# Performance work log

Measured on AMD Instinct MI355X. Metric: run time of the kernel, lower is better.

## Reference

```python
import jax, jax.numpy as jnp
import numpy as np

IMG_H, IMG_W = 800, 1216
STRIDE = 16
SIZES = (128.0, 256.0, 512.0)
RATIOS = (0.5, 1.0, 2.0)
NMS_THRESH = 0.7
MIN_SIZE = 16.0
PRE_NMS = 6000   # testing mode
POST_NMS = 300   # testing mode


def _base_anchors():
    # torchvision-style: ratio = h/w, anchors centered at origin, xyxy
    base = []
    for s in SIZES:
        for r in RATIOS:
            hr = np.sqrt(r)
            w, h = s / hr, s * hr
            base.append([-w / 2.0, -h / 2.0, w / 2.0, h / 2.0])
    return jnp.asarray(np.array(base, dtype=np.float32))  # [A,4]


def _anchors(H, W):
    base = _base_anchors()                                  # [A,4]
    sx = jnp.arange(W, dtype=jnp.float32) * STRIDE
    sy = jnp.arange(H, dtype=jnp.float32) * STRIDE
    shift_x, shift_y = jnp.meshgrid(sx, sy)                 # [H,W] each
    shifts = jnp.stack([shift_x, shift_y, shift_x, shift_y], axis=-1)
    # row-major over (h, w), anchors innermost -> matches permute(0,2,3,1) layout
    return (shifts.reshape(-1, 1, 4) + base[None]).reshape(-1, 4)  # [H*W*A,4]


def _conv(x, w, b, pad):
    y = jax.lax.conv_general_dilated(x, w, (1, 1), pad,
                                     dimension_numbers=('NCHW', 'OIHW', 'NCHW'))
    return y + b[None, :, None, None]


def _decode(deltas, anchors):
    wa = anchors[:, 2] - anchors[:, 0]
    ha = anchors[:, 3] - anchors[:, 1]
    cxa = anchors[:, 0] + 0.5 * wa
    cya = anchors[:, 1] + 0.5 * ha
    cx = deltas[:, 0] * wa + cxa
    cy = deltas[:, 1] * ha + cya
    w = jnp.exp(deltas[:, 2]) * wa
    h = jnp.exp(deltas[:, 3]) * ha
    return jnp.stack([cx - 0.5 * w, cy - 0.5 * h, cx + 0.5 * w, cy + 0.5 * h], axis=-1)


def _nms(boxes, scores):
    # boxes: [N,4] sorted by descending score; greedy IoU-suppression NMS
    N = boxes.shape[0]
    areas = (boxes[:, 2] - boxes[:, 0]) * (boxes[:, 3] - boxes[:, 1])

    def body(i, st):
        sup, kidx, kval = st
        avail = jnp.where(sup, -jnp.inf, scores)
        j = jnp.argmax(avail)
        valid = avail[j] > -jnp.inf
        b = boxes[j]
        ix1 = jnp.maximum(b[0], boxes[:, 0])
        iy1 = jnp.maximum(b[1], boxes[:, 1])
        ix2 = jnp.minimum(b[2], boxes[:, 2])
        iy2 = jnp.minimum(b[3], boxes[:, 3])
        inter = jnp.clip(ix2 - ix1, 0.0) * jnp.clip(iy2 - iy1, 0.0)
        union = areas[j] + areas - inter
        iou = jnp.where(union > 0, inter / union, 0.0)
        sup2 = (sup | (iou > NMS_THRESH)).at[j].set(True)
        sup = jnp.where(valid, sup2, sup.at[j].set(True))
        return sup, kidx.at[i].set(j), kval.at[i].set(valid)

    sup0 = jnp.zeros((N,), jnp.bool_)
    _, kidx, kval = jax.lax.fori_loop(
        0, POST_NMS, body,
        (sup0, jnp.zeros((POST_NMS,), jnp.int32), jnp.zeros((POST_NMS,), jnp.bool_)))
    # fixed-size output [POST_NMS,4]; invalid slots zeroed
    return boxes[kidx] * kval[:, None].astype(boxes.dtype)


def setup_inputs() -> dict:
    key = jax.random.key(0)
    ks = jax.random.split(key, 4)
    return {
        'features': jax.random.normal(ks[0], (8, 512, 50, 76), jnp.float32),
        'conv_w': 0.01 * jax.random.normal(ks[1], (512, 512, 3, 3), jnp.float32),
        'conv_b': jnp.zeros((512,), jnp.float32),
        'cls_w': 0.01 * jax.random.normal(ks[2], (9, 512, 1, 1), jnp.float32),
        'cls_b': jnp.zeros((9,), jnp.float32),
        'box_w': 0.01 * jax.random.normal(ks[3], (36, 512, 1, 1), jnp.float32),
        'box_b': jnp.zeros((36,), jnp.float32),
    }


def reference(features, conv_w, conv_b, cls_w, cls_b, box_w, box_b):
    B, _, H, W = features.shape
    t = jax.nn.relu(_conv(features, conv_w, conv_b, 'SAME'))
    obj = _conv(t, cls_w, cls_b, 'VALID')                     # [B,A,H,W]
    objectness = jnp.transpose(obj, (0, 2, 3, 1)).reshape(B, -1)        # [B,N]
    bd = _conv(t, box_w, box_b, 'VALID')                      # [B,4A,H,W]
    bbox_deltas = jnp.transpose(bd, (0, 2, 3, 1)).reshape(B, -1, 4)     # [B,N,4]
    anchors = _anchors(H, W)                                  # [N,4]

    def per_image(scores, deltas):
        props = _decode(deltas, anchors)
        props = jnp.stack([jnp.clip(props[:, 0], 0.0, IMG_W),
                           jnp.clip(props[:, 1], 0.0, IMG_H),
                           jnp.clip(props[:, 2], 0.0, IMG_W),
                           jnp.clip(props[:, 3], 0.0, IMG_H)], axis=-1)
        keep = ((props[:, 2] - props[:, 0]) >= MIN_SIZE) & \
               ((props[:, 3] - props[:, 1]) >= MIN_SIZE)
        s = jnp.where(keep, scores, -jnp.inf)  # small boxes never selected
        top_s, top_i = jax.lax.top_k(s, PRE_NMS)
        return _nms(props[top_i], top_s)

    proposals = jax.vmap(per_image)(objectness, bbox_deltas)  # [B,POST_NMS,4]
    return proposals, objectness, bbox_deltas
```

## Files before the change

### kernel.cpp

```cpp
#include <hip/hip_runtime.h>
#include <stdint.h>
#include <math.h>

typedef unsigned int u32;
typedef unsigned long long u64;
typedef double d4 __attribute__((ext_vector_type(4)));
typedef _Float16 h8 __attribute__((ext_vector_type(8)));
typedef float f32x16 __attribute__((ext_vector_type(16)));

#define NPX    3800
#define NANCH  34200
#define NSEL   6000
#define NOUT   300
#define NPXP   4160

#define OFF_T        0ull
#define OFF_WTH      62259200ull
#define OFF_WTL      66977792ull
#define OFF_BOXES    71696384ull
#define OFF_ITEMS    76073984ull
#define OFF_FSPH     78262784ull
#define OFF_FSPL     112341504ull
#define WS_NEED_F16  146551296ull
#define OFF_PART     OFF_FSPH
#define WS_NEED_SPLITK (OFF_PART + 43776000ull)

#define GLL16(gsrc, ldst) \
    __builtin_amdgcn_global_load_lds((const __attribute__((address_space(1))) void*)(gsrc), \
                                     (__attribute__((address_space(3))) void*)(ldst), 16, 0, 0)

__global__ __launch_bounds__(256) void zero_kernel(float4* __restrict__ p, unsigned n) {
    unsigned i = blockIdx.x * 256u + threadIdx.x;
    const unsigned stride = gridDim.x * 256u;
    const float4 z = make_float4(0.f, 0.f, 0.f, 0.f);
    for (; i < n; i += stride) p[i] = z;
}

__global__ __launch_bounds__(256) void wsplit_kernel(const float* __restrict__ cw,
                                                     _Float16* __restrict__ wh,
                                                     _Float16* __restrict__ wl) {
    int o = blockIdx.x * 256 + threadIdx.x;
    if (o >= 9 * 512 * 512) return;
    int ci = o & 511;
    int co = (o >> 9) & 511;
    int kk = o >> 18;
    float v = cw[(((co << 9) + ci) * 9) + kk] * 1024.0f;
    _Float16 h = (_Float16)v;
    float r = v - (float)h;
    wh[o] = h;
    wl[o] = (_Float16)r;
}

__global__ __launch_bounds__(256) void fsplit_kernel(const float* __restrict__ feat,
                                                     _Float16* __restrict__ fh,
                                                     _Float16* __restrict__ fl) {
    const int b = blockIdx.z, ci0 = blockIdx.y << 5, p0 = blockIdx.x << 6;
    const int tid = threadIdx.x;
    __shared__ __align__(16) _Float16 shh[64][32];
    __shared__ __align__(16) _Float16 shl[64][32];
    {
        const int r = tid >> 3, xg = tid & 7;
        const int p = p0 + (xg << 3);
        float v[8];
        if (p < NPX) {
            const float* sp = feat + ((size_t)(b * 512 + ci0 + r)) * NPX + p;
            #pragma unroll
            for (int j = 0; j < 8; ++j) v[j] = sp[j];
        } else {
            #pragma unroll
            for (int j = 0; j < 8; ++j) v[j] = 0.f;
        }
        #pragma unroll
        for (int j = 0; j < 8; ++j) {
            float s = v[j] * 512.0f;
            _Float16 h = (_Float16)s;
            float rr = s - (float)h;
            shh[(xg << 3) + j][r] = h;
            shl[(xg << 3) + j][r] = (_Float16)rr;
        }
    }
    __syncthreads();
    {
        const int px = tid >> 2, cg = tid & 3;
        const int p = p0 + px;
        if (p < NPX) {
            const int yy = p / 76, xx = p - yy * 76;
            const size_t dst = ((size_t)b * NPXP + (size_t)((yy + 1) * 80 + xx + 2)) * 512
                             + ci0 + (cg << 3);
            *(h8*)(fh + dst) = *(const h8*)&shh[px][cg << 3];
            *(h8*)(fl + dst) = *(const h8*)&shl[px][cg << 3];
        }
    }
}

__global__ __launch_bounds__(256, 2) void conv3x3_f16_kernel(
    const _Float16* __restrict__ fh, const _Float16* __restrict__ fl,
    const _Float16* __restrict__ wh, const _Float16* __restrict__ wl,
    const float* __restrict__ bias, float* __restrict__ t)
{
    const int id  = blockIdx.x;
    const int b   = id & 7;
    const int g   = id >> 3;
    const int co0 = (g & 3) << 7;
    const int pt0 = (g >> 2) << 7;
    const int tid = threadIdx.x;
    const int w   = tid >> 6;
    const int l   = tid & 63;
    const int wm  = w >> 1, wn = w & 1;
    const int ln  = l & 31, lk = l >> 5;

    __shared__ __align__(16) _Float16 S[2][16][512];

    const _Float16* sb[4];
    u32 ldof[4];
    const long long fbase = (long long)b * NPXP + pt0;
    #pragma unroll
    for (int i = 0; i < 4; ++i) {
        const int ti = (w << 2) + i;
        ldof[i] = (u32)(ti * 1024 + l * 16);
        if (ti < 8) {
            const int mtile = ti >> 1, hl = ti & 1;
            sb[i] = (hl ? wl : wh) + ((long long)(co0 + (mtile << 5) + ln) << 9) + (lk << 3);
        } else {
            const int tj = ti - 8;
            const int ntile = tj >> 1, hl = tj & 1;
            sb[i] = (hl ? fl : fh) + ((fbase + (ntile << 5) + ln) << 9) + (lk << 3);
        }
    }
    char* lbase = (char*)&S[0][0][0];

    auto stage = [&](int q, int db) {
        const int kk  = q >> 5;
        const int ci0 = (q & 31) << 4;
        long long off;
        if (w < 2) {
            off = ((long long)kk << 18) + ci0;
        } else {
            const int kd = (kk * 11) >> 5;
            const int s  = kd * 77 + kk - 81;
            off = ((long long)s << 9) + ci0;
        }
        char* ld = lbase + (db << 14);
        #pragma unroll
        for (int i = 0; i < 4; ++i)
            GLL16(sb[i] + off, ld + ldof[i]);
    };

    f32x16 acc[2][2], l2[2][2];
    #pragma unroll
    for (int i = 0; i < 2; ++i)
        #pragma unroll
        for (int j = 0; j < 2; ++j)
            #pragma unroll
            for (int gg = 0; gg < 16; ++gg) { acc[i][j][gg] = 0.0f; l2[i][j][gg] = 0.0f; }

    stage(0, 0);
    __syncthreads();

    const int ao = l << 3;

    for (int q = 0; q < 288; ++q) {
        const int db = q & 1;
        if (q < 287) stage(q + 1, db ^ 1);
        const _Float16* Sq = &S[db][0][0];
        h8 Ah[2], Al[2], Bh[2], Bl[2];
        #pragma unroll
        for (int i = 0; i < 2; ++i) {
            const int mtile = (wm << 1) + i;
            const int ntile = (wn << 1) + i;
            Ah[i] = *(const h8*)(Sq + ((mtile << 1) + 0) * 512 + ao);
            Al[i] = *(const h8*)(Sq + ((mtile << 1) + 1) * 512 + ao);
            Bh[i] = *(const h8*)(Sq + ((8 + (ntile << 1)) + 0) * 512 + ao);
            Bl[i] = *(const h8*)(Sq + ((8 + (ntile << 1)) + 1) * 512 + ao);
        }
        #pragma unroll
        for (int i = 0; i < 2; ++i)
            #pragma unroll
            for (int j = 0; j < 2; ++j) {
                acc[i][j] = __builtin_amdgcn_mfma_f32_32x32x16_f16(Ah[i], Bh[j], acc[i][j], 0, 0, 0);
                acc[i][j] = __builtin_amdgcn_mfma_f32_32x32x16_f16(Ah[i], Bl[j], acc[i][j], 0, 0, 0);
                acc[i][j] = __builtin_amdgcn_mfma_f32_32x32x16_f16(Al[i], Bh[j], acc[i][j], 0, 0, 0);
            }
        if ((q & 7) == 7) {
            #pragma unroll
            for (int i = 0; i < 2; ++i)
                #pragma unroll
                for (int j = 0; j < 2; ++j) {
                    l2[i][j] += acc[i][j];
                    #pragma unroll
                    for (int gg = 0; gg < 16; ++gg) acc[i][j][gg] = 0.0f;
                }
        }
        if (q < 287) __syncthreads();
    }

    int rcp[16];
    {
        h8 pa, pb;
        #pragma unroll
        for (int j = 0; j < 8; ++j) { pa[j] = (_Float16)(float)ln; pb[j] = (_Float16)0.0625f; }
        f32x16 pr, pc;
        #pragma unroll
        for (int gg = 0; gg < 16; ++gg) { pr[gg] = 0.0f; pc[gg] = 0.0f; }
        pr = __builtin_amdgcn_mfma_f32_32x32x16_f16(pa, pb, pr, 0, 0, 0);
        pc = __builtin_amdgcn_mfma_f32_32x32x16_f16(pb, pa, pc, 0, 0, 0);
        #pragma unroll
        for (int gg = 0; gg < 16; ++gg)
            rcp[gg] = ((int)(pr[gg] + 0.5f)) | (((int)(pc[gg] + 0.5f)) << 8);
    }

    const double dsc = 1.0 / 524288.0;
    #pragma unroll
    for (int i = 0; i < 2; ++i) {
        #pragma unroll
        for (int j = 0; j < 2; ++j) {
            #pragma unroll
            for (int gg = 0; gg < 16; ++gg) {
                const int row = rcp[gg] & 255;
                const int col = rcp[gg] >> 8;
                const int co  = co0 + (wm << 6) + (i << 5) + row;
                const int pp  = pt0 + (wn << 6) + (j << 5) + col;
                const int yy  = pp / 80;
                const int xx  = pp - yy * 80;
                if (yy >= 1 && yy < 51 && xx >= 2 && xx < 78) {
                    const double v = (double)l2[i][j][gg] * dsc + (double)bias[co];
                    t[((size_t)(b * 512 + co)) * NPX + (yy - 1) * 76 + (xx - 2)]
                        = (float)(v > 0.0 ? v : 0.0);
                }
            }
        }
    }
}

__global__ __launch_bounds__(1024) void wtrans_kernel(const float* __restrict__ cw,
                                                      float* __restrict__ wt) {
    int o = blockIdx.x * 1024 + threadIdx.x;
    if (o >= 512*512*9) return;
    int co = o & 511;
    int ci = (o >> 9) & 511;
    int kk = o >> 18;
    wt[o] = cw[((co << 9) + ci) * 9 + kk];
}

__global__ __launch_bounds__(256, 2) void conv3x3_mfma_kernel(const float* __restrict__ feat,
                                                              const float* __restrict__ wt,
                                                              const float* __restrict__ bias,
                                                              float* __restrict__ t) {
    const int b   = blockIdx.z;
    const int co0 = blockIdx.y << 7;
    const int px0 = blockIdx.x << 6;
    const int tid = threadIdx.x;
    const int w    = tid >> 6;
    const int l    = tid & 63;
    const int quad = l >> 4;
    const int lc   = l & 15;

    __shared__ double BsF[2][1024];

    int rr[4], cc[4];
    {
        d4 pzr = {0.0, 0.0, 0.0, 0.0};
        d4 pzc = {0.0, 0.0, 0.0, 0.0};
        double paM = (double)lc;
        double pbN = (double)lc;
        pzr = __builtin_amdgcn_mfma_f64_16x16x4f64(paM, 1.0, pzr, 0, 0, 0);
        pzc = __builtin_amdgcn_mfma_f64_16x16x4f64(1.0, pbN, pzc, 0, 0, 0);
        #pragma unroll
        for (int g = 0; g < 4; ++g) {
            rr[g] = (((int)pzr[g]) >> 2) & 15;
            cc[g] = (((int)pzc[g]) >> 2) & 15;
        }
    }

    d4 acc[2][4];
    #pragma unroll
    for (int i = 0; i < 2; ++i)
        #pragma unroll
        for (int j = 0; j < 4; ++j) acc[i][j] = (d4){0.0, 0.0, 0.0, 0.0};

    const float* featb = feat + (size_t)b * 512 * NPX;

    const int b_quad = (tid >> 4) & 3;
    const int b_pxl  = ((tid >> 6) << 4) | (tid & 15);
    const int p      = px0 + b_pxl;
    const int py     = p / 76;
    const int px     = p - py * 76;
    const bool pvalid = (p < NPX);

    float vaf[8], vbf[4];
    double a_cur[8];

    auto loadA = [&](int q, float* va) {
        int kk  = q >> 5;
        int ci0 = (q & 31) << 4;
        const float* ap = wt + (((size_t)(kk * 512 + ci0 + quad)) << 9)
                             + co0 + (w << 5) + lc;
        #pragma unroll
        for (int ks = 0; ks < 4; ++ks) {
            va[ks * 2 + 0] = ap[(ks << 11)];
            va[ks * 2 + 1] = ap[(ks << 11) + 16];
        }
    };
    auto loadB = [&](int q, float* vb) {
        int kk  = q >> 5;
        int ci0 = (q & 31) << 4;
        int kd = kk / 3;
        int dy = kd - 1, dx = kk - kd * 3 - 1;
        int iy = py + dy, ix = px + dx;
        bool ok = pvalid && ((unsigned)iy < 50u) && ((unsigned)ix < 76u);
        if (ok) {
            const float* bp = featb + (size_t)(ci0 + b_quad) * NPX + iy * 76 + ix;
            #pragma unroll
            for (int j = 0; j < 4; ++j) vb[j] = bp[(size_t)(j << 2) * NPX];
        } else {
            vb[0] = vb[1] = vb[2] = vb[3] = 0.0f;
        }
    };

    loadA(0, vaf); loadB(0, vbf);
    #pragma unroll
    for (int j = 0; j < 4; ++j) BsF[0][tid + (j << 8)] = (double)vbf[j];
    #pragma unroll
    for (int j = 0; j < 8; ++j) a_cur[j] = (double)vaf[j];
    __syncthreads();

    for (int q = 0; q < 288; ++q) {
        const int cur = q & 1;
        if (q < 287) { loadA(q + 1, vaf); loadB(q + 1, vbf); }
        const double* bb = BsF[cur];
        #pragma unroll
        for (int ks = 0; ks < 4; ++ks) {
            const double* bp = bb + (ks << 8);
            double a0 = a_cur[ks * 2], a1 = a_cur[ks * 2 + 1];
            #pragma unroll
            for (int nt = 0; nt < 4; ++nt) {
                double bv = bp[(nt << 6) + l];
                acc[0][nt] = __builtin_amdgcn_mfma_f64_16x16x4f64(a0, bv, acc[0][nt], 0, 0, 0);
                acc[1][nt] = __builtin_amdgcn_mfma_f64_16x16x4f64(a1, bv, acc[1][nt], 0, 0, 0);
            }
        }
        if (q < 287) {
            #pragma unroll
            for (int j = 0; j < 4; ++j) BsF[cur ^ 1][tid + (j << 8)] = (double)vbf[j];
            #pragma unroll
            for (int j = 0; j < 8; ++j) a_cur[j] = (double)vaf[j];
            __syncthreads();
        }
    }

    #pragma unroll
    for (int mt = 0; mt < 2; ++mt) {
        #pragma unroll
        for (int g = 0; g < 4; ++g) {
            int co = co0 + (w << 5) + (mt << 4) + rr[g];
            double bs = (double)bias[co];
            float* row = t + ((size_t)b * 512 + co) * NPX;
            #pragma unroll
            for (int nt = 0; nt < 4; ++nt) {
                int pp = px0 + (nt << 4) + cc[g];
                if (pp < NPX) {
                    double v = acc[mt][nt][g] + bs;
                    row[pp] = (float)(v > 0.0 ? v : 0.0);
                }
            }
        }
    }
}

__global__ __launch_bounds__(64) void heads_partial_kernel(const float* __restrict__ t,
                                                           const float* __restrict__ cls_w,
                                                           const float* __restrict__ box_w,
                                                           double* __restrict__ part) {
    const int b = blockIdx.y, c = blockIdx.z;
    const int p = blockIdx.x * 64 + threadIdx.x;
    if (p >= NPX) return;
    const float* tb = t + ((size_t)b * 512 + c * 128) * NPX + p;

    double ac[9]  = {};
    double ab[36] = {};
    for (int ci = 0; ci < 128; ++ci) {
        double tv = (double)tb[(size_t)ci * NPX];
        int cw = c * 128 + ci;
        #pragma unroll
        for (int o = 0; o < 9;  ++o) ac[o] = fma((double)cls_w[o * 512 + cw], tv, ac[o]);
        #pragma unroll
        for (int o = 0; o < 36; ++o) ab[o] = fma((double)box_w[o * 512 + cw], tv, ab[o]);
    }
    double* dst = part + ((size_t)(c * 8 + b) * 45) * NPX + p;
    #pragma unroll
    for (int o = 0; o < 9;  ++o) dst[(size_t)o * NPX] = ac[o];
    #pragma unroll
    for (int o = 0; o < 36; ++o) dst[(size_t)(9 + o) * NPX] = ab[o];
}

__device__ __forceinline__ void decode_px(int b, int p, const double* s45,
                                          const float* cls_b, const float* box_b,
                                          float* out_obj, float* out_del,
                                          float* boxes, u64* items) {
    float* ob = out_obj + (size_t)b * NANCH + (size_t)p * 9;
    float* dl = out_del + (size_t)b * NANCH * 4 + (size_t)p * 36;
    const int yy = p / 76, xx = p - yy * 76;

    #pragma unroll
    for (int a = 0; a < 9; ++a) {
        double s  = s45[a] + (double)cls_b[a];
        ob[a] = (float)s;
        double d0 = s45[9 + 4*a + 0] + (double)box_b[4*a+0];
        double d1 = s45[9 + 4*a + 1] + (double)box_b[4*a+1];
        double d2 = s45[9 + 4*a + 2] + (double)box_b[4*a+2];
        double d3 = s45[9 + 4*a + 3] + (double)box_b[4*a+3];
        dl[4*a+0] = (float)d0; dl[4*a+1] = (float)d1;
        dl[4*a+2] = (float)d2; dl[4*a+3] = (float)d3;

        int si = a / 3, ri = a - si * 3;
        double sz = (si == 0) ? 128.0 : ((si == 1) ? 256.0 : 512.0);
        double hr = (ri == 0) ? 0.7071067811865476 : ((ri == 1) ? 1.0 : 1.4142135623730951);
        float bx2f = (float)(sz / hr * 0.5);
        float by2f = (float)(sz * hr * 0.5);

        double sx = (double)(xx * 16), sy = (double)(yy * 16);
        double x1 = sx - (double)bx2f, x2 = sx + (double)bx2f;
        double y1 = sy - (double)by2f, y2 = sy + (double)by2f;

        double wa = x2 - x1, ha = y2 - y1;
        double cxa = x1 + 0.5 * wa, cya = y1 + 0.5 * ha;
        double cx = d0 * wa + cxa, cy = d1 * ha + cya;
        double w  = exp(d2) * wa,  h  = exp(d3) * ha;

        double px1 = cx - 0.5 * w, py1 = cy - 0.5 * h;
        double px2 = cx + 0.5 * w, py2 = cy + 0.5 * h;
        px1 = fmin(fmax(px1, 0.0), 1216.0);
        py1 = fmin(fmax(py1, 0.0), 800.0);
        px2 = fmin(fmax(px2, 0.0), 1216.0);
        py2 = fmin(fmax(py2, 0.0), 800.0);

        bool keep = ((px2 - px1) >= 16.0) && ((py2 - py1) >= 16.0);
        double se = keep ? s : -INFINITY;

        u64 ubits = (u64)__double_as_longlong(se);
        u64 ka = (ubits >> 63) ? ~ubits : (ubits | 0x8000000000000000ull);
        u64 kd = ~ka;
        int n = p * 9 + a;
        items[(size_t)b * NANCH + n] = (kd & ~0xFFFFull) | (u64)(u32)n;
        *(float4*)(boxes + ((size_t)b * NANCH + n) * 4) =
            make_float4((float)px1, (float)py1, (float)px2, (float)py2);
    }
}

__global__ __launch_bounds__(64) void reduce_decode_kernel(const double* __restrict__ part,
                                                           const float* __restrict__ cls_b,
                                                           const float* __restrict__ box_b,
                                                           float* __restrict__ out_obj,
                                                           float* __restrict__ out_del,
                                                           float* __restrict__ boxes,
                                                           u64* __restrict__ items) {
    const int b = blockIdx.y;
    const int p = blockIdx.x * 64 + threadIdx.x;
    if (p >= NPX) return;
    double s45[45];
    #pragma unroll
    for (int o = 0; o < 45; ++o) {
        double s = part[((size_t)(0 * 8 + b) * 45 + o) * NPX + p];
        s += part[((size_t)(1 * 8 + b) * 45 + o) * NPX + p];
        s += part[((size_t)(2 * 8 + b) * 45 + o) * NPX + p];
        s += part[((size_t)(3 * 8 + b) * 45 + o) * NPX + p];
        s45[o] = s;
    }
    decode_px(b, p, s45, cls_b, box_b, out_obj, out_del, boxes, items);
}

__global__ __launch_bounds__(256) void heads_decode_kernel(const float* __restrict__ t,
                                                           const float* __restrict__ cls_w,
                                                           const float* __restrict__ cls_b,
                                                           const float* __restrict__ box_w,
                                                           const float* __restrict__ box_b,
                                                           float* __restrict__ out_obj,
                                                           float* __restrict__ out_del,
                                                           float* __restrict__ boxes,
                                                           u64* __restrict__ items) {
    const int b = blockIdx.y;
    const int p = blockIdx.x * 256 + threadIdx.x;
    if (p >= NPX) return;
    const float* tb = t + (size_t)b * 512 * NPX + p;
    double s45[45];
    #pragma unroll
    for (int o = 0; o < 45; ++o) s45[o] = 0.0;
    for (int ci = 0; ci < 512; ++ci) {
        double tv = (double)tb[(size_t)ci * NPX];
        #pragma unroll
        for (int o = 0; o < 9;  ++o) s45[o]     = fma((double)cls_w[o * 512 + ci], tv, s45[o]);
        #pragma unroll
        for (int o = 0; o < 36; ++o) s45[9 + o] = fma((double)box_w[o * 512 + ci], tv, s45[9 + o]);
    }
    decode_px(b, p, s45, cls_b, box_b, out_obj, out_del, boxes, items);
}

__device__ __forceinline__ bool iou_gt(float4 A, float4 B, float areaA, float areaB) {
    float ix1 = fmaxf(A.x, B.x), iy1 = fmaxf(A.y, B.y);
    float ix2 = fminf(A.z, B.z), iy2 = fminf(A.w, B.w);
    float iw = fmaxf(ix2 - ix1, 0.0f), ih = fmaxf(iy2 - iy1, 0.0f);
    float inter = iw * ih;
    float uni = areaA + areaB - inter;
    float iou = (uni > 0.0f) ? (inter / uni) : 0.0f;
    return iou > 0.7f;
}

__global__ __launch_bounds__(1024) void topk_nms_kernel(const u64* __restrict__ items,
                                                        const float* __restrict__ boxes,
                                                        float* __restrict__ out) {
    extern __shared__ u64 buf[];
    u32* hist = (u32*)buf;
    u32* scan = hist + 4096;
    u32* scal = hist + 5120;

    const int b   = blockIdx.x;
    const int tid = threadIdx.x;
    const u64* it = items + (size_t)b * NANCH;

    #pragma unroll
    for (int i = 0; i < 4; ++i) hist[tid * 4 + i] = 0;
    __syncthreads();
    for (int i = tid; i < NANCH; i += 1024)
        atomicAdd(&hist[(u32)(it[i] >> 52)], 1);
    __syncthreads();

    u32 B1, cum1;
    {
        u32 c0 = hist[tid*4], c1 = hist[tid*4+1], c2 = hist[tid*4+2], c3 = hist[tid*4+3];
        u32 S = c0 + c1 + c2 + c3;
        scan[tid] = S;
        __syncthreads();
        for (int off = 1; off < 1024; off <<= 1) {
            u32 v = (tid >= off) ? scan[tid - off] : 0;
            __syncthreads();
            scan[tid] += v;
            __syncthreads();
        }
        u32 excl = scan[tid] - S;
        const u32 target = 5999;
        if (target >= excl && target < excl + S) {
            u32 pfx = excl, bidx, cum;
            if      (target < pfx + c0)           { bidx = tid*4;   cum = pfx; }
            else if (target < pfx + c0 + c1)      { bidx = tid*4+1; cum = pfx + c0; }
            else if (target < pfx + c0 + c1 + c2) { bidx = tid*4+2; cum = pfx + c0 + c1; }
            else                                  { bidx = tid*4+3; cum = pfx + c0 + c1 + c2; }
            scal[0] = bidx; scal[1] = cum;
        }
    }
    __syncthreads();
    B1 = scal[0]; cum1 = scal[1];
    __syncthreads();

    #pragma unroll
    for (int i = 0; i < 4; ++i) hist[tid * 4 + i] = 0;
    __syncthreads();
    for (int i = tid; i < NANCH; i += 1024) {
        u64 v = it[i];
        if ((u32)(v >> 52) == B1)
            atomicAdd(&hist[(u32)(v >> 40) & 0xFFF], 1);
    }
    __syncthreads();

    u32 B2;
    {
        u32 c0 = hist[tid*4], c1 = hist[tid*4+1], c2 = hist[tid*4+2], c3 = hist[tid*4+3];
        u32 S = c0 + c1 + c2 + c3;
        scan[tid] = S;
        __syncthreads();
        for (int off = 1; off < 1024; off <<= 1) {
            u32 v = (tid >= off) ? scan[tid - off] : 0;
            __syncthreads();
            scan[tid] += v;
            __syncthreads();
        }
        u32 excl = scan[tid] - S;
        const u32 target = 5999 - cum1;
        if (target >= excl && target < excl + S) {
            u32 pfx = excl, bidx;
            if      (target < pfx + c0)           bidx = tid*4;
            else if (target < pfx + c0 + c1)      bidx = tid*4+1;
            else if (target < pfx + c0 + c1 + c2) bidx = tid*4+2;
            else                                  bidx = tid*4+3;
            scal[2] = bidx;
        }
    }
    __syncthreads();
    B2 = scal[2];
    const u32 T = ((B1 << 12) | B2) + 1;
    __syncthreads();

    for (int i = tid; i < 8192; i += 1024) buf[i] = ~0ull;
    __syncthreads();
    u32* cnt = (u32*)&buf[8191];
    if (tid == 0) *cnt = 0;
    __syncthreads();
    for (int i = tid; i < NANCH; i += 1024) {
        u64 v = it[i];
        if ((u32)(v >> 40) < T) {
            u32 pos = atomicAdd(cnt, 1);
            if (pos < 8191) buf[pos] = v;
        }
    }
    __syncthreads();
    if (tid == 0) buf[8191] = ~0ull;
    __syncthreads();

    for (int size = 2; size <= 8192; size <<= 1) {
        for (int stride = size >> 1; stride > 0; stride >>= 1) {
            #pragma unroll
            for (int v = 0; v < 4; ++v) {
                int idx = tid + (v << 10);
                int i = 2 * idx - (idx & (stride - 1));
                int j = i + stride;
                bool up = ((i & size) == 0);
                u64 x = buf[i], y = buf[j];
                if ((x > y) == up) { buf[i] = y; buf[j] = x; }
            }
            __syncthreads();
        }
    }

    float4 bx6[6]; u32 dead6[6];
    #pragma unroll
    for (int s = 0; s < 6; ++s) {
        int r = tid + (s << 10);
        u64 v = buf[r];
        bool dd = (r >= NSEL) || ((u32)(v >> 32) >= 0xFFF00000u);
        float4 bb = make_float4(0.f, 0.f, 0.f, 0.f);
        if (!dd) {
            u32 n = (u32)(v & 0xFFFFull);
            bb = *(const float4*)(boxes + ((size_t)b * NANCH + n) * 4);
        }
        bx6[s] = bb;
        dead6[s] = dd ? 1u : 0u;
    }
    __syncthreads();

    float4* candbox = (float4*)buf;
    u64*    wmask   = (u64*)(buf + 2560);
    float4* accb    = (float4*)(buf + 3072);
    u32*    cntp    = (u32*)(buf + 3712);
    if (tid == 0) *cntp = 0;
    __syncthreads();

    for (int s = 0; s < 6; ++s) {
        int count = (int)*cntp;
        if (count >= NOUT) break;
        float4 mb = bx6[s];
        float  ma = (mb.z - mb.x) * (mb.w - mb.y);
        bool dd = dead6[s] != 0;
        for (int a2 = 0; a2 < count && !dd; ++a2) {
            float4 abx = accb[a2];
            if (iou_gt(mb, abx, ma, (abx.z - abx.x) * (abx.w - abx.y))) dd = true;
        }
        candbox[tid] = mb;
        u64 bal = __ballot(!dd);
        if ((tid & 63) == 0) wmask[tid >> 6] = bal;
        __syncthreads();
        if (tid < 64) {
            int cnt2 = count;
            for (int w2 = 0; w2 < 16 && cnt2 < NOUT; ++w2) {
                u64 mm = wmask[w2];
                while (mm != 0 && cnt2 < NOUT) {
                    int bit = __ffsll(mm) - 1;
                    mm &= (mm - 1);
                    float4 cb = candbox[(w2 << 6) + bit];
                    float  ca = (cb.z - cb.x) * (cb.w - cb.y);
                    bool okc = true;
                    for (int base = count; base < cnt2 && okc; base += 64) {
                        int idx = base + tid;
                        bool bad = false;
                        if (idx < cnt2) {
                            float4 abx = accb[idx];
                            bad = iou_gt(cb, abx, ca, (abx.z - abx.x) * (abx.w - abx.y));
                        }
                        if (__any(bad)) okc = false;
                    }
                    if (okc) {
                        if (tid == 0) accb[cnt2] = cb;
                        cnt2++;
                    }
                }
            }
            if (tid == 0) *cntp = (u32)cnt2;
        }
        __syncthreads();
    }

    int fin = (int)*cntp;
    for (int r = tid; r < NOUT; r += 1024) {
        float4 v = (r < fin) ? accb[r] : make_float4(0.f, 0.f, 0.f, 0.f);
        *(float4*)(out + ((size_t)b * NOUT + r) * 4) = v;
    }
}

extern "C" void kernel_launch(void* const* d_in, const int* in_sizes, int n_in,
                              void* d_out, int out_size, void* d_ws, size_t ws_size,
                              hipStream_t stream) {
    const float* feat   = (const float*)d_in[0];
    const float* conv_w = (const float*)d_in[1];
    const float* conv_b = (const float*)d_in[2];
    const float* cls_w  = (const float*)d_in[3];
    const float* cls_b  = (const float*)d_in[4];
    const float* box_w  = (const float*)d_in[5];
    const float* box_b  = (const float*)d_in[6];

    float* out       = (float*)d_out;
    float* out_props = out;
    float* out_obj   = out + 9600;
    float* out_del   = out + 9600 + 273600;

    char* ws = (char*)d_ws;
    float*    t     = (float*)(ws + OFF_T);
    _Float16* wth   = (_Float16*)(ws + OFF_WTH);
    _Float16* wtl   = (_Float16*)(ws + OFF_WTL);
    float*    wtf   = (float*)(ws + OFF_WTH);
    float*    boxes = (float*)(ws + OFF_BOXES);
    u64*      items = (u64*)(ws + OFF_ITEMS);
    _Float16* fsph  = (_Float16*)(ws + OFF_FSPH);
    _Float16* fspl  = (_Float16*)(ws + OFF_FSPL);
    double*   part  = (double*)(ws + OFF_PART);

    if (ws_size >= WS_NEED_F16) {
        hipLaunchKernelGGL(zero_kernel, dim3(2048), dim3(256), 0, stream,
                           (float4*)(ws + OFF_FSPH), 4259840u);
        hipLaunchKernelGGL(wsplit_kernel, dim3(9216), dim3(256), 0, stream,
                           conv_w, wth, wtl);
        hipLaunchKernelGGL(fsplit_kernel, dim3(60, 16, 8), dim3(256), 0, stream,
                           feat, fsph, fspl);
        hipLaunchKernelGGL(conv3x3_f16_kernel, dim3(1024), dim3(256), 0, stream,
                           fsph, fspl, wth, wtl, conv_b, t);
    } else {
        hipLaunchKernelGGL(wtrans_kernel, dim3(2304), dim3(1024), 0, stream, conv_w, wtf);
        hipLaunchKernelGGL(conv3x3_mfma_kernel, dim3(60, 4, 8), dim3(256), 0, stream,
                           feat, wtf, conv_b, t);
    }
    if (ws_size >= WS_NEED_SPLITK) {
        hipLaunchKernelGGL(heads_partial_kernel, dim3(60, 8, 4), dim3(64), 0, stream,
                           t, cls_w, box_w, part);
        hipLaunchKernelGGL(reduce_decode_kernel, dim3(60, 8), dim3(64), 0, stream,
                           part, cls_b, box_b, out_obj, out_del, boxes, items);
    } else {
        hipLaunchKernelGGL(heads_decode_kernel, dim3(15, 8), dim3(256), 0, stream,
                           t, cls_w, cls_b, box_w, box_b, out_obj, out_del, boxes, items);
    }
    hipLaunchKernelGGL(topk_nms_kernel, dim3(8), dim3(1024), 65536, stream,
                       items, boxes, out_props);
}
```

Measured before the change: 1.193 ms.

## Enlarge conv tile to 512 threads with 5-slot LDS ring and deeper prefetch

```diff
diff --git a/kernel.cpp b/kernel.cpp
--- a/kernel.cpp
+++ b/kernel.cpp
@@ -93,7 +93,7 @@
     }
 }
 
-__global__ __launch_bounds__(256, 2) void conv3x3_f16_kernel(
+__global__ __launch_bounds__(512, 2) void conv3x3_f16_kernel(
     const _Float16* __restrict__ fh, const _Float16* __restrict__ fl,
     const _Float16* __restrict__ wh, const _Float16* __restrict__ wl,
     const float* __restrict__ bias, float* __restrict__ t)
@@ -101,49 +101,48 @@
     const int id  = blockIdx.x;
     const int b   = id & 7;
     const int g   = id >> 3;
-    const int co0 = (g & 3) << 7;
-    const int pt0 = (g >> 2) << 7;
+    const int co0 = (g >> 4) << 7;
+    const int pt0 = (g & 15) << 8;
     const int tid = threadIdx.x;
     const int w   = tid >> 6;
     const int l   = tid & 63;
-    const int wm  = w >> 1, wn = w & 1;
+    const int wm  = w >> 2, wn = w & 3;
     const int ln  = l & 31, lk = l >> 5;
 
-    __shared__ __align__(16) _Float16 S[2][16][512];
-
-    const _Float16* sb[4];
-    u32 ldof[4];
+    __shared__ __align__(16) _Float16 S[5][24][512];
+
+    const _Float16* sb[3];
+    u32 ldof[3];
+    bool isA[3];
     const long long fbase = (long long)b * NPXP + pt0;
     #pragma unroll
-    for (int i = 0; i < 4; ++i) {
-        const int ti = (w << 2) + i;
+    for (int i = 0; i < 3; ++i) {
+        const int ti = w * 3 + i;
         ldof[i] = (u32)(ti * 1024 + l * 16);
+        isA[i] = (ti < 8);
         if (ti < 8) {
-            const int mtile = ti >> 1, hl = ti & 1;
-            sb[i] = (hl ? wl : wh) + ((long long)(co0 + (mtile << 5) + ln) << 9) + (lk << 3);
+            const int mt = ti >> 1, hl = ti & 1;
+            sb[i] = (hl ? wl : wh) + ((long long)(co0 + (mt << 5) + ln) << 9) + (lk << 3);
         } else {
-            const int tj = ti - 8;
-            const int ntile = tj >> 1, hl = tj & 1;
-            sb[i] = (hl ? fl : fh) + ((fbase + (ntile << 5) + ln) << 9) + (lk << 3);
+            const int tj = ti - 8, nt = tj >> 1, hl = tj & 1;
+            sb[i] = (hl ? fl : fh) + ((fbase + (nt << 5) + ln) << 9) + (lk << 3);
         }
     }
     char* lbase = (char*)&S[0][0][0];
 
-    auto stage = [&](int q, int db) {
+    auto stage = [&](int q, int slot) {
         const int kk  = q >> 5;
         const int ci0 = (q & 31) << 4;
-        long long off;
-        if (w < 2) {
-            off = ((long long)kk << 18) + ci0;
-        } else {
-            const int kd = (kk * 11) >> 5;
-            const int s  = kd * 77 + kk - 81;
-            off = ((long long)s << 9) + ci0;
-        }
-        char* ld = lbase + (db << 14);
-        #pragma unroll
-        for (int i = 0; i < 4; ++i)
+        const long long offA = ((long long)kk << 18) + ci0;
+        const int kd = (kk * 11) >> 5;
+        const int s  = kd * 77 + kk - 81;
+        const long long offB = ((long long)s << 9) + ci0;
+        char* ld = lbase + slot * 24576;
+        #pragma unroll
+        for (int i = 0; i < 3; ++i) {
+            const long long off = isA[i] ? offA : offB;
             GLL16(sb[i] + off, ld + ldof[i]);
+        }
     };
 
     f32x16 acc[2][2], l2[2][2];
@@ -154,34 +153,68 @@
             #pragma unroll
             for (int gg = 0; gg < 16; ++gg) { acc[i][j][gg] = 0.0f; l2[i][j][gg] = 0.0f; }
 
-    stage(0, 0);
-    __syncthreads();
-
     const int ao = l << 3;
 
-    for (int q = 0; q < 288; ++q) {
-        const int db = q & 1;
-        if (q < 287) stage(q + 1, db ^ 1);
-        const _Float16* Sq = &S[db][0][0];
-        h8 Ah[2], Al[2], Bh[2], Bl[2];
+    auto readFrags = [&](int slot, h8* Ah, h8* Al, h8* Bh, h8* Bl) {
+        const _Float16* Sq = (const _Float16*)(lbase + slot * 24576);
         #pragma unroll
         for (int i = 0; i < 2; ++i) {
-            const int mtile = (wm << 1) + i;
-            const int ntile = (wn << 1) + i;
-            Ah[i] = *(const h8*)(Sq + ((mtile << 1) + 0) * 512 + ao);
-            Al[i] = *(const h8*)(Sq + ((mtile << 1) + 1) * 512 + ao);
-            Bh[i] = *(const h8*)(Sq + ((8 + (ntile << 1)) + 0) * 512 + ao);
-            Bl[i] = *(const h8*)(Sq + ((8 + (ntile << 1)) + 1) * 512 + ao);
-        }
-        #pragma unroll
-        for (int i = 0; i < 2; ++i)
-            #pragma unroll
-            for (int j = 0; j < 2; ++j) {
-                acc[i][j] = __builtin_amdgcn_mfma_f32_32x32x16_f16(Ah[i], Bh[j], acc[i][j], 0, 0, 0);
-                acc[i][j] = __builtin_amdgcn_mfma_f32_32x32x16_f16(Ah[i], Bl[j], acc[i][j], 0, 0, 0);
-                acc[i][j] = __builtin_amdgcn_mfma_f32_32x32x16_f16(Al[i], Bh[j], acc[i][j], 0, 0, 0);
-            }
-        if ((q & 7) == 7) {
+            const int mt = (wm << 1) + i, nt = (wn << 1) + i;
+            Ah[i] = *(const h8*)(Sq + (((mt << 1) + 0) << 9) + ao);
+            Al[i] = *(const h8*)(Sq + (((mt << 1) + 1) << 9) + ao);
+            Bh[i] = *(const h8*)(Sq + ((8 + (nt << 1) + 0) << 9) + ao);
+            Bl[i] = *(const h8*)(Sq + ((8 + (nt << 1) + 1) << 9) + ao);
+        }
+    };
+
+    stage(0, 0); stage(1, 1); stage(2, 2);
+    asm volatile("s_waitcnt vmcnt(3)" ::: "memory");
+    __builtin_amdgcn_sched_barrier(0);
+    __builtin_amdgcn_s_barrier();
+
+    int s0 = 0;
+    for (int F = 0; F < 144; ++F) {
+        const int q0 = F << 1;
+        int s1 = s0 + 1; if (s1 >= 5) s1 -= 5;
+        int s3 = s0 + 3; if (s3 >= 5) s3 -= 5;
+        int s4 = s0 + 4; if (s4 >= 5) s4 -= 5;
+        if (q0 + 3 < 288) stage(q0 + 3, s3);
+        if (q0 + 4 < 288) stage(q0 + 4, s4);
+
+        h8 A0h[2], A0l[2], B0h[2], B0l[2];
+        h8 A1h[2], A1l[2], B1h[2], B1l[2];
+        readFrags(s0, A0h, A0l, B0h, B0l);
+        __builtin_amdgcn_s_setprio(1);
+        acc[0][0] = __builtin_amdgcn_mfma_f32_32x32x16_f16(A0h[0], B0h[0], acc[0][0], 0, 0, 0);
+        acc[0][0] = __builtin_amdgcn_mfma_f32_32x32x16_f16(A0h[0], B0l[0], acc[0][0], 0, 0, 0);
+        acc[0][0] = __builtin_amdgcn_mfma_f32_32x32x16_f16(A0l[0], B0h[0], acc[0][0], 0, 0, 0);
+        acc[0][1] = __builtin_amdgcn_mfma_f32_32x32x16_f16(A0h[0], B0h[1], acc[0][1], 0, 0, 0);
+        acc[0][1] = __builtin_amdgcn_mfma_f32_32x32x16_f16(A0h[0], B0l[1], acc[0][1], 0, 0, 0);
+        acc[0][1] = __builtin_amdgcn_mfma_f32_32x32x16_f16(A0l[0], B0h[1], acc[0][1], 0, 0, 0);
+        __builtin_amdgcn_s_setprio(0);
+        readFrags(s1, A1h, A1l, B1h, B1l);
+        __builtin_amdgcn_s_setprio(1);
+        acc[1][0] = __builtin_amdgcn_mfma_f32_32x32x16_f16(A0h[1], B0h[0], acc[1][0], 0, 0, 0);
+        acc[1][0] = __builtin_amdgcn_mfma_f32_32x32x16_f16(A0h[1], B0l[0], acc[1][0], 0, 0, 0);
+        acc[1][0] = __builtin_amdgcn_mfma_f32_32x32x16_f16(A0l[1], B0h[0], acc[1][0], 0, 0, 0);
+        acc[1][1] = __builtin_amdgcn_mfma_f32_32x32x16_f16(A0h[1], B0h[1], acc[1][1], 0, 0, 0);
+        acc[1][1] = __builtin_amdgcn_mfma_f32_32x32x16_f16(A0h[1], B0l[1], acc[1][1], 0, 0, 0);
+        acc[1][1] = __builtin_amdgcn_mfma_f32_32x32x16_f16(A0l[1], B0h[1], acc[1][1], 0, 0, 0);
+        acc[0][0] = __builtin_amdgcn_mfma_f32_32x32x16_f16(A1h[0], B1h[0], acc[0][0], 0, 0, 0);
+        acc[0][0] = __builtin_amdgcn_mfma_f32_32x32x16_f16(A1h[0], B1l[0], acc[0][0], 0, 0, 0);
+        acc[0][0] = __builtin_amdgcn_mfma_f32_32x32x16_f16(A1l[0], B1h[0], acc[0][0], 0, 0, 0);
+        acc[0][1] = __builtin_amdgcn_mfma_f32_32x32x16_f16(A1h[0], B1h[1], acc[0][1], 0, 0, 0);
+        acc[0][1] = __builtin_amdgcn_mfma_f32_32x32x16_f16(A1h[0], B1l[1], acc[0][1], 0, 0, 0);
+        acc[0][1] = __builtin_amdgcn_mfma_f32_32x32x16_f16(A1l[0], B1h[1], acc[0][1], 0, 0, 0);
+        acc[1][0] = __builtin_amdgcn_mfma_f32_32x32x16_f16(A1h[1], B1h[0], acc[1][0], 0, 0, 0);
+        acc[1][0] = __builtin_amdgcn_mfma_f32_32x32x16_f16(A1h[1], B1l[0], acc[1][0], 0, 0, 0);
+        acc[1][0] = __builtin_amdgcn_mfma_f32_32x32x16_f16(A1l[1], B1h[0], acc[1][0], 0, 0, 0);
+        acc[1][1] = __builtin_amdgcn_mfma_f32_32x32x16_f16(A1h[1], B1h[1], acc[1][1], 0, 0, 0);
+        acc[1][1] = __builtin_amdgcn_mfma_f32_32x32x16_f16(A1h[1], B1l[1], acc[1][1], 0, 0, 0);
+        acc[1][1] = __builtin_amdgcn_mfma_f32_32x32x16_f16(A1l[1], B1h[1], acc[1][1], 0, 0, 0);
+        __builtin_amdgcn_s_setprio(0);
+
+        if (((q0 + 1) & 7) == 7) {
             #pragma unroll
             for (int i = 0; i < 2; ++i)
                 #pragma unroll
@@ -191,7 +224,14 @@
                     for (int gg = 0; gg < 16; ++gg) acc[i][j][gg] = 0.0f;
                 }
         }
-        if (q < 287) __syncthreads();
+
+        if (F < 143) {
+            if (q0 + 4 < 288) { asm volatile("s_waitcnt vmcnt(3)" ::: "memory"); }
+            else              { asm volatile("s_waitcnt vmcnt(0)" ::: "memory"); }
+            __builtin_amdgcn_sched_barrier(0);
+            __builtin_amdgcn_s_barrier();
+        }
+        s0 += 2; if (s0 >= 5) s0 -= 5;
     }
 
     int rcp[16];
@@ -728,7 +768,7 @@
                            conv_w, wth, wtl);
         hipLaunchKernelGGL(fsplit_kernel, dim3(60, 16, 8), dim3(256), 0, stream,
                            feat, fsph, fspl);
-        hipLaunchKernelGGL(conv3x3_f16_kernel, dim3(1024), dim3(256), 0, stream,
+        hipLaunchKernelGGL(conv3x3_f16_kernel, dim3(512), dim3(512), 0, stream,
                            fsph, fspl, wth, wtl, conv_b, t);
     } else {
         hipLaunchKernelGGL(wtrans_kernel, dim3(2304), dim3(1024), 0, stream, conv_w, wtf);
```

After: 1.130 ms. 1.06x faster.
